# Optimization experiments

Measured on AMD Instinct MI355X. Metric: run time of the kernel, lower is better.

## Reference

```python
import jax, jax.numpy as jnp
import numpy as np

IN_FEATURES = 4096
OUT_FEATURES = 4096
SPARSE_RATIO = 0.1
NNZ = int(IN_FEATURES * OUT_FEATURES * SPARSE_RATIO)  # 1677721
N_COLS = 4096  # x is (out_features, N); bias broadcast requires N == out_features


def setup_inputs() -> dict:
    key = jax.random.key(0)
    k_x, k_r, k_c, k_v, k_b = jax.random.split(key, 5)
    x = jax.random.normal(k_x, (OUT_FEATURES, N_COLS), dtype=jnp.float32)
    rows = jax.random.randint(k_r, (NNZ,), 0, IN_FEATURES, dtype=jnp.int32)
    cols = jax.random.randint(k_c, (NNZ,), 0, OUT_FEATURES, dtype=jnp.int32)
    vals = jax.random.normal(k_v, (NNZ,), dtype=jnp.float32)
    bias = jax.random.normal(k_b, (OUT_FEATURES,), dtype=jnp.float32)
    return {"x": x, "rows": rows, "cols": cols, "vals": vals, "bias": bias}


def reference(x, rows, cols, vals, bias):
    # Scatter the COO weight into its dense form once (duplicate coords
    # accumulate, matching sparse COO coalescing semantics), then do a
    # dense GEMM: y = W @ x + bias. Same math as torch.sparse.mm.
    W = jnp.zeros((IN_FEATURES, OUT_FEATURES), dtype=x.dtype).at[rows, cols].add(vals)
    return W @ x + bias  # (in_features, N) + (out_features,) broadcast on last axis
```

## Files before the change

kernel.cpp:

```cpp
#include <hip/hip_runtime.h>
#include <hip/hip_bf16.h>
#include <stdint.h>

#define MDIM 4096
#define NDIM 4096
#define KDIM 4096

typedef float f32x4 __attribute__((ext_vector_type(4)));
typedef __bf16 bf16x8 __attribute__((ext_vector_type(8)));
typedef short s16x8 __attribute__((ext_vector_type(8)));


__device__ __forceinline__ unsigned short f2bf(float x) {
  union { float f; unsigned u; } v; v.f = x;
  return (unsigned short)((v.u + 0x7fffu + ((v.u >> 16) & 1u)) >> 16);
}
__device__ __forceinline__ float bf2f(unsigned short b) {
  union { unsigned u; float f; } v; v.u = ((unsigned)b) << 16;
  return v.f;
}

__device__ __forceinline__ void cas_add_bf16(unsigned short* addr2, unsigned short bits, int hi) {
  unsigned* word = (unsigned*)addr2;
  unsigned shift = hi ? 16u : 0u;
  float v = bf2f(bits);
  unsigned old = *word, assumed;
  do {
    assumed = old;
    unsigned short cur = (unsigned short)(assumed >> shift);
    unsigned short upd = f2bf(bf2f(cur) + v);
    unsigned next = (assumed & ~(0xffffu << shift)) | ((unsigned)upd << shift);
    if (next == assumed) break;
    old = atomicCAS(word, assumed, next);
  } while (old != assumed);
}

template <typename T>
__device__ __forceinline__ auto pk_add_impl(T* p, T v, int)
    -> decltype(unsafeAtomicAdd(p, v), void()) {
  unsafeAtomicAdd(p, v);
}
template <typename T>
__device__ __forceinline__ void pk_add_impl(T* p, T v, long) {
  union { T t; unsigned u; } c; c.t = v;
  unsigned short lo = (unsigned short)(c.u & 0xffffu);
  unsigned short hi16 = (unsigned short)(c.u >> 16);
  if (lo) cas_add_bf16((unsigned short*)p, lo, 0);
  if (hi16) cas_add_bf16((unsigned short*)p, hi16, 1);
}

__device__ __forceinline__ void atomic_bf16_add(unsigned short* base2, unsigned short bits, int hi) {
  __hip_bfloat162_raw raw;
  raw.x = hi ? (unsigned short)0 : bits;
  raw.y = hi ? bits : (unsigned short)0;
  __hip_bfloat162 v(raw);
  pk_add_impl((__hip_bfloat162*)base2, v, 0);
}

__global__ __launch_bounds__(256) void prep_kernel(const int* __restrict__ rows,
                                                   const int* __restrict__ cols,
                                                   const float* __restrict__ vals, int nnz,
                                                   int scBlocks,
                                                   unsigned short* __restrict__ Wpk,
                                                   const float* __restrict__ x,
                                                   short* __restrict__ Xpk) {
  int b = blockIdx.x, tid = threadIdx.x;
  if (b < scBlocks) {
    int i = b * 256 + tid;
    if (i >= nnz) return;
    int m = rows[i], k = cols[i];
    unsigned short bits = f2bf(vals[i]);
    size_t chunk = ((((size_t)(m >> 7) * 128 + (k >> 5)) * 8 + ((m >> 4) & 7)) * 64) +
                   (((k >> 3) & 3) * 16 + (m & 15));
    size_t idx = chunk * 8 + (k & 7);
    atomic_bf16_add(&Wpk[idx & ~(size_t)1], bits, (int)(idx & 1));
  } else {
    __shared__ float tile[32 * 65];
    int pb = b - scBlocks;
    int n0 = (pb & 63) * 64, k0 = (pb >> 6) * 32;
#pragma unroll
    for (int r = 0; r < 8; r++) {
      int elem = r * 256 + tid;
      int kk = elem >> 6, nn = elem & 63;
      tile[kk * 65 + nn] = x[(size_t)(k0 + kk) * NDIM + n0 + nn];
    }
    __syncthreads();
    int region = tid >> 6, lane = tid & 63;
    int kh = lane >> 4, nl = region * 16 + (lane & 15);
    s16x8 v;
#pragma unroll
    for (int j = 0; j < 8; j++) v[j] = (short)f2bf(tile[(kh * 8 + j) * 65 + nl]);
    int f = region;
    f = ((n0 & 127) >> 4) + region;
    size_t chunk = (((size_t)(n0 >> 7) * 128 + (k0 >> 5)) * 8 + f) * 64 + lane;
    *(s16x8*)&Xpk[chunk * 8] = v;
  }
}

__global__ __launch_bounds__(256) void gemm_kernel(const short* __restrict__ A,
                                                   const short* __restrict__ Bt,
                                                   const float* __restrict__ bias,
                                                   float* __restrict__ C) {
  __shared__ __align__(16) short sA[2][128 * 32];
  __shared__ __align__(16) short sB[2][128 * 32];
  int tid = threadIdx.x, lane = tid & 63, wave = tid >> 6;
  int wr = wave >> 1, wc = wave & 1;
  int m16 = lane & 15, quad = lane >> 4;
  int rowBase = blockIdx.y * 128, colBase = blockIdx.x * 128;

  f32x4 acc[4][4];
#pragma unroll
  for (int i = 0; i < 4; i++)
#pragma unroll
    for (int j = 0; j < 4; j++) acc[i][j] = f32x4{0.f, 0.f, 0.f, 0.f};

  const short* aSrc[2];
  const short* bSrc[2];
  int ldsDst[2];
#pragma unroll
  for (int s = 0; s < 2; s++) {
    int f = wave + s * 4;
    aSrc[s] = A + ((size_t)blockIdx.y * 128 * 8 + f) * 512 + lane * 8;
    bSrc[s] = Bt + ((size_t)blockIdx.x * 128 * 8 + f) * 512 + lane * 8;
    ldsDst[s] = f * 512;
  }

#pragma unroll
  for (int s = 0; s < 2; s++) {
    __builtin_amdgcn_global_load_lds(
        (const __attribute__((address_space(1))) void*)aSrc[s],
        (__attribute__((address_space(3))) void*)&sA[0][ldsDst[s]], 16, 0, 0);
    __builtin_amdgcn_global_load_lds(
        (const __attribute__((address_space(1))) void*)bSrc[s],
        (__attribute__((address_space(3))) void*)&sB[0][ldsDst[s]], 16, 0, 0);
  }

#pragma unroll 2
  for (int it = 0; it < 128; it++) {
    int buf = it & 1, nxt = buf ^ 1;
    int tnext = (it + 1) & 127;
#pragma unroll
    for (int s = 0; s < 2; s++) {
      __builtin_amdgcn_global_load_lds(
          (const __attribute__((address_space(1))) void*)(aSrc[s] + (size_t)tnext * 4096),
          (__attribute__((address_space(3))) void*)&sA[nxt][ldsDst[s]], 16, 0, 0);
      __builtin_amdgcn_global_load_lds(
          (const __attribute__((address_space(1))) void*)(bSrc[s] + (size_t)tnext * 4096),
          (__attribute__((address_space(3))) void*)&sB[nxt][ldsDst[s]], 16, 0, 0);
    }
    __builtin_amdgcn_s_waitcnt(0x0F74);
    __builtin_amdgcn_s_barrier();

    bf16x8 a[4], b[4];
#pragma unroll
    for (int i = 0; i < 4; i++)
      a[i] = *(const bf16x8*)&sA[buf][((wr * 4 + i) * 64 + lane) * 8];
#pragma unroll
    for (int j = 0; j < 4; j++)
      b[j] = *(const bf16x8*)&sB[buf][((wc * 4 + j) * 64 + lane) * 8];
#pragma unroll
    for (int i = 0; i < 4; i++)
#pragma unroll
      for (int j = 0; j < 4; j++)
        acc[i][j] = __builtin_amdgcn_mfma_f32_16x16x32_bf16(a[i], b[j], acc[i][j], 0, 0, 0);

    __builtin_amdgcn_s_waitcnt(0xC07F);
    __builtin_amdgcn_s_barrier();
  }
  __builtin_amdgcn_s_waitcnt(0x0F70);

#pragma unroll
  for (int j = 0; j < 4; j++) {
    int col = colBase + wc * 64 + j * 16 + m16;
    float bv = bias[col];
#pragma unroll
    for (int i = 0; i < 4; i++) {
      int row0 = rowBase + wr * 64 + i * 16 + quad * 4;
      f32x4 v = acc[i][j];
#pragma unroll
      for (int r = 0; r < 4; r++) C[(size_t)(row0 + r) * NDIM + col] = v[r] + bv;
    }
  }
}

extern "C" void kernel_launch(void* const* d_in, const int* in_sizes, int n_in,
                              void* d_out, int out_size, void* d_ws, size_t ws_size,
                              hipStream_t stream) {
  const float* x = (const float*)d_in[0];
  const int* rows = (const int*)d_in[1];
  const int* cols = (const int*)d_in[2];
  const float* vals = (const float*)d_in[3];
  const float* bias = (const float*)d_in[4];
  int nnz = in_sizes[1];
  float* y = (float*)d_out;

  char* ws = (char*)d_ws;
  unsigned short* Wpk = (unsigned short*)ws;
  short* Xpk = (short*)(ws + (32u << 20));

  int scBlocks = (nnz + 255) / 256;
  int pxBlocks = (NDIM / 64) * (KDIM / 32);

  hipMemsetAsync(Wpk, 0, (size_t)MDIM * KDIM * sizeof(short), stream);
  prep_kernel<<<scBlocks + pxBlocks, 256, 0, stream>>>(rows, cols, vals, nnz, scBlocks,
                                                       Wpk, x, Xpk);
  gemm_kernel<<<dim3(NDIM / 128, MDIM / 128), 256, 0, stream>>>((const short*)Wpk, Xpk, bias, y);
}
```

Before: 366.1 us.

## Enlarge GEMM tile to 256x256 with 8 waves and 4-stage LDS pipeline

The GEMM block tile grows from 128x128 to 256x256, with 512 threads and each wave computing a 128x64 output. LDS buffering goes from 2 to 4 stages with a prefetch distance of 3. Loads for B are interleaved between the two MFMA halves, and s_setprio raises wave priority during the MFMA sections. The aim is more operand reuse per global load and better overlap of memory with compute. The cost is 128 KB of LDS per block and 128 accumulator registers per thread, which limits occupancy, and a grid of only 256 blocks.

```diff
diff --git a/kernel.cpp b/kernel.cpp
--- a/kernel.cpp
+++ b/kernel.cpp
@@ -90,93 +90,106 @@
     s16x8 v;
 #pragma unroll
     for (int j = 0; j < 8; j++) v[j] = (short)f2bf(tile[(kh * 8 + j) * 65 + nl]);
-    int f = region;
-    f = ((n0 & 127) >> 4) + region;
+    int f = ((n0 & 127) >> 4) + region;
     size_t chunk = (((size_t)(n0 >> 7) * 128 + (k0 >> 5)) * 8 + f) * 64 + lane;
     *(s16x8*)&Xpk[chunk * 8] = v;
   }
 }
 
-__global__ __launch_bounds__(256) void gemm_kernel(const short* __restrict__ A,
-                                                   const short* __restrict__ Bt,
-                                                   const float* __restrict__ bias,
-                                                   float* __restrict__ C) {
-  __shared__ __align__(16) short sA[2][128 * 32];
-  __shared__ __align__(16) short sB[2][128 * 32];
-  int tid = threadIdx.x, lane = tid & 63, wave = tid >> 6;
-  int wr = wave >> 1, wc = wave & 1;
+
+#define GLOAD16(gp, lp)                                              \
+  __builtin_amdgcn_global_load_lds(                                  \
+      (const __attribute__((address_space(1))) void*)(gp),           \
+      (__attribute__((address_space(3))) void*)(lp), 16, 0, 0)
+
+__global__ __launch_bounds__(512, 2) void gemm_kernel(const short* __restrict__ A,
+                                                      const short* __restrict__ Bt,
+                                                      const float* __restrict__ bias,
+                                                      float* __restrict__ C) {
+  __shared__ __align__(16) short sA[4][8192];
+  __shared__ __align__(16) short sB[4][8192];
+
+  int tid = threadIdx.x, lane = tid & 63, w = tid >> 6;
+  int wr = w >> 2, wc = w & 3;
   int m16 = lane & 15, quad = lane >> 4;
-  int rowBase = blockIdx.y * 128, colBase = blockIdx.x * 128;
-
-  f32x4 acc[4][4];
-#pragma unroll
-  for (int i = 0; i < 4; i++)
+  int by = blockIdx.y, bx = blockIdx.x;
+
+  f32x4 acc[8][4];
+#pragma unroll
+  for (int i = 0; i < 8; i++)
 #pragma unroll
     for (int j = 0; j < 4; j++) acc[i][j] = f32x4{0.f, 0.f, 0.f, 0.f};
 
   const short* aSrc[2];
   const short* bSrc[2];
-  int ldsDst[2];
+  int ldsOff[2];
 #pragma unroll
   for (int s = 0; s < 2; s++) {
-    int f = wave + s * 4;
-    aSrc[s] = A + ((size_t)blockIdx.y * 128 * 8 + f) * 512 + lane * 8;
-    bSrc[s] = Bt + ((size_t)blockIdx.x * 128 * 8 + f) * 512 + lane * 8;
-    ldsDst[s] = f * 512;
-  }
-
-#pragma unroll
-  for (int s = 0; s < 2; s++) {
-    __builtin_amdgcn_global_load_lds(
-        (const __attribute__((address_space(1))) void*)aSrc[s],
-        (__attribute__((address_space(3))) void*)&sA[0][ldsDst[s]], 16, 0, 0);
-    __builtin_amdgcn_global_load_lds(
-        (const __attribute__((address_space(1))) void*)bSrc[s],
-        (__attribute__((address_space(3))) void*)&sB[0][ldsDst[s]], 16, 0, 0);
-  }
-
-#pragma unroll 2
-  for (int it = 0; it < 128; it++) {
-    int buf = it & 1, nxt = buf ^ 1;
-    int tnext = (it + 1) & 127;
-#pragma unroll
-    for (int s = 0; s < 2; s++) {
-      __builtin_amdgcn_global_load_lds(
-          (const __attribute__((address_space(1))) void*)(aSrc[s] + (size_t)tnext * 4096),
-          (__attribute__((address_space(3))) void*)&sA[nxt][ldsDst[s]], 16, 0, 0);
-      __builtin_amdgcn_global_load_lds(
-          (const __attribute__((address_space(1))) void*)(bSrc[s] + (size_t)tnext * 4096),
-          (__attribute__((address_space(3))) void*)&sB[nxt][ldsDst[s]], 16, 0, 0);
-    }
-    __builtin_amdgcn_s_waitcnt(0x0F74);
+    aSrc[s] = A + ((size_t)(2 * by + s) * 128 * 8 + w) * 512 + lane * 8;
+    bSrc[s] = Bt + ((size_t)(2 * bx + s) * 128 * 8 + w) * 512 + lane * 8;
+    ldsOff[s] = (s * 8 + w) * 512 + lane * 8;
+  }
+
+#pragma unroll
+  for (int t = 0; t < 3; t++) {
+    GLOAD16(aSrc[0] + (size_t)t * 4096, &sA[t][ldsOff[0]]);
+    GLOAD16(aSrc[1] + (size_t)t * 4096, &sA[t][ldsOff[1]]);
+    GLOAD16(bSrc[0] + (size_t)t * 4096, &sB[t][ldsOff[0]]);
+    GLOAD16(bSrc[1] + (size_t)t * 4096, &sB[t][ldsOff[1]]);
+  }
+
+  for (int t = 0; t < 128; t++) {
+    int buf = t & 3;
+    int nbuf = (t + 3) & 3;
+    size_t tn = (size_t)((t + 3) & 127) * 4096;
+
+    GLOAD16(aSrc[0] + tn, &sA[nbuf][ldsOff[0]]);
+    GLOAD16(aSrc[1] + tn, &sA[nbuf][ldsOff[1]]);
+    __builtin_amdgcn_s_waitcnt(0x0F7A);
     __builtin_amdgcn_s_barrier();
 
-    bf16x8 a[4], b[4];
-#pragma unroll
-    for (int i = 0; i < 4; i++)
-      a[i] = *(const bf16x8*)&sA[buf][((wr * 4 + i) * 64 + lane) * 8];
-#pragma unroll
-    for (int j = 0; j < 4; j++)
-      b[j] = *(const bf16x8*)&sB[buf][((wc * 4 + j) * 64 + lane) * 8];
-#pragma unroll
-    for (int i = 0; i < 4; i++)
-#pragma unroll
-      for (int j = 0; j < 4; j++)
-        acc[i][j] = __builtin_amdgcn_mfma_f32_16x16x32_bf16(a[i], b[j], acc[i][j], 0, 0, 0);
-
-    __builtin_amdgcn_s_waitcnt(0xC07F);
+    const short* pA = &sA[buf][0];
+    const short* pB = &sB[buf][0];
+    bf16x8 a[8], b[4];
+
+#pragma unroll
+    for (int mi = 0; mi < 4; mi++)
+      a[mi] = *(const bf16x8*)&pA[(wr * 8 + mi) * 512 + lane * 8];
+#pragma unroll
+    for (int nj = 0; nj < 4; nj++)
+      b[nj] = *(const bf16x8*)&pB[((wc >> 1) * 8 + (wc & 1) * 4 + nj) * 512 + lane * 8];
+    __builtin_amdgcn_s_setprio(1);
+#pragma unroll
+    for (int mi = 0; mi < 4; mi++)
+#pragma unroll
+      for (int nj = 0; nj < 4; nj++)
+        acc[mi][nj] = __builtin_amdgcn_mfma_f32_16x16x32_bf16(a[mi], b[nj], acc[mi][nj], 0, 0, 0);
+    __builtin_amdgcn_s_setprio(0);
+
+    GLOAD16(bSrc[0] + tn, &sB[nbuf][ldsOff[0]]);
+    GLOAD16(bSrc[1] + tn, &sB[nbuf][ldsOff[1]]);
+#pragma unroll
+    for (int mi = 4; mi < 8; mi++)
+      a[mi] = *(const bf16x8*)&pA[(wr * 8 + mi) * 512 + lane * 8];
+    __builtin_amdgcn_s_setprio(1);
+#pragma unroll
+    for (int mi = 4; mi < 8; mi++)
+#pragma unroll
+      for (int nj = 0; nj < 4; nj++)
+        acc[mi][nj] = __builtin_amdgcn_mfma_f32_16x16x32_bf16(a[mi], b[nj], acc[mi][nj], 0, 0, 0);
+    __builtin_amdgcn_s_setprio(0);
     __builtin_amdgcn_s_barrier();
   }
   __builtin_amdgcn_s_waitcnt(0x0F70);
 
 #pragma unroll
-  for (int j = 0; j < 4; j++) {
-    int col = colBase + wc * 64 + j * 16 + m16;
+  for (int nj = 0; nj < 4; nj++) {
+    int col = bx * 256 + wc * 64 + nj * 16 + m16;
     float bv = bias[col];
 #pragma unroll
-    for (int i = 0; i < 4; i++) {
-      int row0 = rowBase + wr * 64 + i * 16 + quad * 4;
-      f32x4 v = acc[i][j];
+    for (int mi = 0; mi < 8; mi++) {
+      int row0 = by * 256 + wr * 128 + mi * 16 + quad * 4;
+      f32x4 v = acc[mi][nj];
 #pragma unroll
       for (int r = 0; r < 4; r++) C[(size_t)(row0 + r) * NDIM + col] = v[r] + bv;
     }
@@ -204,5 +217,5 @@
   hipMemsetAsync(Wpk, 0, (size_t)MDIM * KDIM * sizeof(short), stream);
   prep_kernel<<<scBlocks + pxBlocks, 256, 0, stream>>>(rows, cols, vals, nnz, scBlocks,
                                                        Wpk, x, Xpk);
-  gemm_kernel<<<dim3(NDIM / 128, MDIM / 128), 256, 0, stream>>>((const short*)Wpk, Xpk, bias, y);
-}
+  gemm_kernel<<<dim3(NDIM / 256, MDIM / 256), 512, 0, stream>>>((const short*)Wpk, Xpk, bias, y);
+}
```

Result: faster. 352.3 us (-3.8%).
